# Kernel optimization log

Measured on AMD Instinct MI355X. Metric: run time of the kernel, lower is better.

Reference implementation:

```python
import jax, jax.numpy as jnp
import numpy as np

H = 2048      # hidden_size
DM = 4096     # intermediate_size
N = 16        # ssm state size
K = 4         # conv kernel
R = 128       # time_step_rank
B_SZ = 1
L = 1024


def setup_inputs() -> dict:
    key = jax.random.key(0)
    ks = jax.random.split(key, 10)
    s = 0.02
    hidden_states = jax.random.normal(ks[0], (B_SZ, L, H), dtype=jnp.float32)
    W_in = jax.random.normal(ks[1], (2 * DM, H), dtype=jnp.float32) * s
    conv_w = jax.random.normal(ks[2], (DM, 1, K), dtype=jnp.float32) * 0.3
    conv_b = jax.random.normal(ks[3], (DM,), dtype=jnp.float32) * 0.1
    W_x = jax.random.normal(ks[4], (R + 2 * N, DM), dtype=jnp.float32) * s
    W_dt = jax.random.normal(ks[5], (DM, R), dtype=jnp.float32) * s
    b_dt = jax.random.normal(ks[6], (DM,), dtype=jnp.float32) * 0.1
    # A_log init: log(arange(1..N)) broadcast over channels (per __init__)
    A_log = jnp.broadcast_to(jnp.log(jnp.arange(1, N + 1, dtype=jnp.float32))[None, :], (DM, N)).copy()
    D_param = jnp.ones((DM,), dtype=jnp.float32)
    W_out = jax.random.normal(ks[7], (H, DM), dtype=jnp.float32) * s
    return {"hidden_states": hidden_states, "W_in": W_in, "conv_w": conv_w,
            "conv_b": conv_b, "W_x": W_x, "W_dt": W_dt, "b_dt": b_dt,
            "A_log": A_log, "D_param": D_param, "W_out": W_out}


def reference(hidden_states, W_in, conv_w, conv_b, W_x, W_dt, b_dt, A_log, D_param, W_out):
    # in_proj then chunk into hidden / gate (torch chunks dim=1 after transpose)
    proj = hidden_states @ W_in.T                     # [B, L, 2D]
    h, gate = proj[..., :DM], proj[..., DM:]          # each [B, L, D]
    # depthwise causal conv1d, padding K-1 then truncate to L (left-pad == same)
    h_cl = jnp.transpose(h, (0, 2, 1))                # [B, D, L]
    hc = jax.lax.conv_general_dilated(
        h_cl, conv_w, window_strides=(1,), padding=[(K - 1, 0)],
        dimension_numbers=("NCH", "OIH", "NCH"), feature_group_count=DM)
    hc = jax.nn.silu(hc + conv_b[None, :, None])      # [B, D, L]
    hc_ld = jnp.transpose(hc, (0, 2, 1))              # [B, L, D]
    # x_proj -> dt, B, C
    ssm_p = hc_ld @ W_x.T                             # [B, L, R+2N]
    ts, Bm, Cm = ssm_p[..., :R], ssm_p[..., R:R + N], ssm_p[..., R + N:]
    dt = jax.nn.softplus(ts @ W_dt.T + b_dt)          # [B, L, D]
    A = -jnp.exp(A_log)                               # [D, N]
    dA = jnp.exp(dt[:, :, :, None] * A[None, None, :, :])            # [B, L, D, N]
    dBu = dt[:, :, :, None] * Bm[:, :, None, :] * hc_ld[:, :, :, None]  # [B, L, D, N]
    # selective scan over time: state = dA*state + dBu; y = <state, C>
    def step(state, inp):
        dA_t, dBu_t, C_t = inp                        # [B,D,N],[B,D,N],[B,N]
        state = dA_t * state + dBu_t
        y = jnp.einsum("bdn,bn->bd", state, C_t)
        return state, y
    init = jnp.zeros((hidden_states.shape[0], DM, N), dtype=hidden_states.dtype)
    _, ys = jax.lax.scan(step, init,
                         (jnp.swapaxes(dA, 0, 1), jnp.swapaxes(dBu, 0, 1), jnp.swapaxes(Cm, 0, 1)))
    y = jnp.transpose(ys, (1, 0, 2))                  # [B, L, D]
    y = y + hc_ld * D_param[None, None, :]            # skip via D
    y = y * jax.nn.silu(gate)                         # gating
    return y @ W_out.T                                # [B, L, H]
```

## Files before the change

### kernel.cpp

```cpp
#include <hip/hip_runtime.h>
#include <math.h>

#define AS1 __attribute__((address_space(1)))
#define AS3 __attribute__((address_space(3)))

typedef __attribute__((ext_vector_type(8))) short short8;
typedef __attribute__((ext_vector_type(4))) float f32x4;

#define WAITV(n) asm volatile("s_waitcnt vmcnt(" #n ")" ::: "memory")
#define BARRIER() asm volatile("s_barrier" ::: "memory")

static __device__ __forceinline__ unsigned short f2bf(float f) {
    unsigned u = __float_as_uint(f);
    unsigned r = (u + 0x7fffu + ((u >> 16) & 1u)) >> 16;
    return (unsigned short)r;
}

__global__ __launch_bounds__(256) void cvt_f32_bf16(const float* __restrict__ src,
                                                    unsigned short* __restrict__ dst,
                                                    int n4) {
    int i = blockIdx.x * 256 + threadIdx.x;
    int stride = gridDim.x * 256;
    for (; i < n4; i += stride) {
        float4 v = ((const float4*)src)[i];
        ushort4 o;
        o.x = f2bf(v.x); o.y = f2bf(v.y); o.z = f2bf(v.z); o.w = f2bf(v.w);
        ((ushort4*)dst)[i] = o;
    }
}

__global__ __launch_bounds__(256) void cvt_ts(const float* __restrict__ ssmp,
                                              unsigned short* __restrict__ ts) {
    int i = blockIdx.x * 256 + threadIdx.x;
    int t = i >> 5, c4 = (i & 31) * 4;
    float4 v = *(const float4*)&ssmp[t * 160 + c4];
    ushort4 o;
    o.x = f2bf(v.x); o.y = f2bf(v.y); o.z = f2bf(v.z); o.w = f2bf(v.w);
    *(ushort4*)&ts[t * 128 + c4] = o;
}

__global__ __launch_bounds__(256) void conv_silu(const float* __restrict__ h,
                                                 const float* __restrict__ cw,
                                                 const float* __restrict__ cb,
                                                 float* __restrict__ hc_f,
                                                 unsigned short* __restrict__ hc_bf) {
    int idx = blockIdx.x * 256 + threadIdx.x;
    int d = idx & 4095, t = idx >> 12;
    float acc = cb[d];
    float4 w = *(const float4*)&cw[d * 4];
    const float* wp = (const float*)&w;
#pragma unroll
    for (int k = 0; k < 4; ++k) {
        int tt = t + k - 3;
        if (tt >= 0) acc += h[tt * 4096 + d] * wp[k];
    }
    float s = acc / (1.f + __expf(-acc));
    hc_f[idx] = s;
    hc_bf[idx] = f2bf(s);
}

__global__ __launch_bounds__(256) void reduce4(const float* __restrict__ pA,
                                               const float* __restrict__ pB,
                                               float* __restrict__ out, int n4) {
    int i = blockIdx.x * 256 + threadIdx.x;
    int stride = gridDim.x * 256;
    const size_t MN4 = (size_t)1024 * 2048 / 4;
    for (; i < n4; i += stride) {
        float4 a = ((const float4*)pA)[i];
        float4 b = ((const float4*)pA)[i + MN4];
        float4 c = ((const float4*)pB)[i];
        float4 d = ((const float4*)pB)[i + MN4];
        float4 o;
        o.x = (a.x + b.x) + (c.x + d.x);
        o.y = (a.y + b.y) + (c.y + d.y);
        o.z = (a.z + b.z) + (c.z + d.z);
        o.w = (a.w + b.w) + (c.w + d.w);
        ((float4*)out)[i] = o;
    }
}

enum { P_SPLIT = 0, P_PART = 1 };

template <int EPI>
__global__ __launch_bounds__(512, 2)
void gemm8p(const short* __restrict__ A, const short* __restrict__ B,
            float* __restrict__ C0, float* __restrict__ C1,
            int N, int K, int kchunk) {
    __shared__ short lds[3 * 24576];

    const int tid = threadIdx.x;
    const int wv = tid >> 6, ln = tid & 63;
    const int lr = ln & 15, kg = ln >> 4;
    const int wm = wv >> 2, wn = wv & 3;

    const int nwg = gridDim.x;
    const int bid = blockIdx.x;
    const int swz = (bid & 7) * (nwg >> 3) + (bid >> 3);
    const int by = swz & 7, bx = swz >> 3;
    const int m0 = by * 128;
    const int n0 = bx * 256;
    const int kbeg = blockIdx.z * kchunk;
    const int NT = kchunk >> 6;

    f32x4 acc[4][4];
#pragma unroll
    for (int mi = 0; mi < 4; ++mi)
#pragma unroll
        for (int ni = 0; ni < 4; ++ni) acc[mi][ni] = (f32x4){0.f, 0.f, 0.f, 0.f};

    const short* Abase = A + (size_t)m0 * K + kbeg;
    const short* Bbase = B + (size_t)n0 * K + kbeg;

#define STAGE(kt, b)                                                          \
    {                                                                         \
        short* lbase = &lds[(b) * 24576];                                     \
        _Pragma("unroll")                                                     \
        for (int r = 0; r < 2; ++r) {                                         \
            int c = r * 512 + tid;                                            \
            int row = c >> 3, cb8 = (c & 7) << 4;                             \
            int scb = cb8 ^ ((row & 7) << 4);                                 \
            const short* src = Abase + (size_t)row * K + (kt) * 64 + (scb >> 1); \
            short* dst = lbase + (r * 512 + wv * 64) * 8;                     \
            __builtin_amdgcn_global_load_lds((const AS1 void*)src,            \
                                             (AS3 void*)dst, 16, 0, 0);       \
        }                                                                     \
        _Pragma("unroll")                                                     \
        for (int r = 0; r < 4; ++r) {                                         \
            int c = r * 512 + tid;                                            \
            int row = c >> 3, cb8 = (c & 7) << 4;                             \
            int scb = cb8 ^ ((row & 7) << 4);                                 \
            const short* src = Bbase + (size_t)row * K + (kt) * 64 + (scb >> 1); \
            short* dst = lbase + 8192 + (r * 512 + wv * 64) * 8;              \
            __builtin_amdgcn_global_load_lds((const AS1 void*)src,            \
                                             (AS3 void*)dst, 16, 0, 0);       \
        }                                                                     \
    }

    STAGE(0, 0);
    if (NT > 1) STAGE(1, 1);

    for (int kt = 0; kt < NT; ++kt) {
        const int b = kt % 3;
        if (kt + 2 < NT) STAGE(kt + 2, (kt + 2) % 3);
        int ahead = NT - 1 - kt;
        if (ahead > 2) ahead = 2;
        if (ahead == 2) { WAITV(12); } else if (ahead == 1) { WAITV(6); } else { WAITV(0); }
        BARRIER();
        {
            const short* la = &lds[b * 24576];
            const short* lb = la + 8192;
#pragma unroll
            for (int ks = 0; ks < 2; ++ks) {
                short8 av[4], bv[4];
#pragma unroll
                for (int mi = 0; mi < 4; ++mi) {
                    int row = wm * 64 + mi * 16 + lr;
                    int col = (ks * 32 + kg * 8) ^ ((row & 7) << 3);
                    av[mi] = *(const short8*)&la[row * 64 + col];
                }
#pragma unroll
                for (int ni = 0; ni < 4; ++ni) {
                    int row = wn * 64 + ni * 16 + lr;
                    int col = (ks * 32 + kg * 8) ^ ((row & 7) << 3);
                    bv[ni] = *(const short8*)&lb[row * 64 + col];
                }
                __builtin_amdgcn_s_setprio(1);
#pragma unroll
                for (int mi = 0; mi < 4; ++mi)
#pragma unroll
                    for (int ni = 0; ni < 4; ++ni)
                        acc[mi][ni] = __builtin_amdgcn_mfma_f32_16x16x32_bf16(
                            av[mi], bv[ni], acc[mi][ni], 0, 0, 0);
                __builtin_amdgcn_s_setprio(0);
            }
        }
        BARRIER();
    }
#undef STAGE

#pragma unroll
    for (int mi = 0; mi < 4; ++mi) {
        int crow0 = m0 + wm * 64 + mi * 16 + kg * 4;
#pragma unroll
        for (int ni = 0; ni < 4; ++ni) {
            int ccol = n0 + wn * 64 + ni * 16 + lr;
#pragma unroll
            for (int i = 0; i < 4; ++i) {
                float v = acc[mi][ni][i];
                size_t crow = (size_t)(crow0 + i);
                if constexpr (EPI == P_SPLIT) {
                    if (ccol < 4096) C0[crow * 4096 + ccol] = v;
                    else C1[crow * 4096 + (ccol - 4096)] = v;
                } else {
                    float* Cz = (blockIdx.z < 2 ? C0 : C1) +
                                (size_t)(blockIdx.z & 1) * 1024 * 2048;
                    Cz[crow * N + ccol] = v;
                }
            }
        }
    }
}

enum { EPI_PLAIN = 0, EPI_SPLIT = 1, EPI_ATOMIC = 2, EPI_SOFTPLUS = 3 };

template <int BM, int EPI>
__global__ __launch_bounds__(256)
void gemm_bt(const short* __restrict__ A, const short* __restrict__ B,
             float* __restrict__ C, float* __restrict__ C2,
             const float* __restrict__ bias,
             int M, int N, int K, int ldc, int kcLen) {
    __shared__ short A_lds[BM * 32];
    __shared__ short B_lds[128 * 32];
    const int tid = threadIdx.x;
    const int wv = tid >> 6, ln = tid & 63;
    const int lr = ln & 15, kg = ln >> 4;
    const int m0 = blockIdx.y * BM;
    const int n0 = blockIdx.x * 128;
    const int kbeg = blockIdx.z * kcLen;
    const int kend = kbeg + kcLen;
    const int wm = wv >> 1, wn = wv & 1;
    constexpr int MR = BM / 32;

    f32x4 acc[MR][4];
#pragma unroll
    for (int mi = 0; mi < MR; ++mi)
#pragma unroll
        for (int ni = 0; ni < 4; ++ni) acc[mi][ni] = (f32x4){0.f, 0.f, 0.f, 0.f};

    const int arow = tid >> 2;
    const int kq8 = (tid & 3) * 8;

    for (int k0 = kbeg; k0 < kend; k0 += 32) {
#pragma unroll
        for (int r = 0; r < BM / 64; ++r) {
            const short* srcA = A + (size_t)(m0 + r * 64 + arow) * K + (k0 + kq8);
            short* dstA = &A_lds[(r * 64 + wv * 16) * 32];
            __builtin_amdgcn_global_load_lds((const AS1 void*)srcA, (AS3 void*)dstA, 16, 0, 0);
        }
#pragma unroll
        for (int r = 0; r < 2; ++r) {
            int brow = n0 + r * 64 + arow;
            if (brow > N - 1) brow = N - 1;
            const short* srcB = B + (size_t)brow * K + (k0 + kq8);
            short* dstB = &B_lds[(r * 64 + wv * 16) * 32];
            __builtin_amdgcn_global_load_lds((const AS1 void*)srcB, (AS3 void*)dstB, 16, 0, 0);
        }
        __syncthreads();

        short8 av[MR], bv[4];
#pragma unroll
        for (int mi = 0; mi < MR; ++mi)
            av[mi] = *(const short8*)&A_lds[(wm * (BM / 2) + mi * 16 + lr) * 32 + kg * 8];
#pragma unroll
        for (int ni = 0; ni < 4; ++ni)
            bv[ni] = *(const short8*)&B_lds[(wn * 64 + ni * 16 + lr) * 32 + kg * 8];
#pragma unroll
        for (int mi = 0; mi < MR; ++mi)
#pragma unroll
            for (int ni = 0; ni < 4; ++ni)
                acc[mi][ni] = __builtin_amdgcn_mfma_f32_16x16x32_bf16(av[mi], bv[ni], acc[mi][ni], 0, 0, 0);
        __syncthreads();
    }

#pragma unroll
    for (int mi = 0; mi < MR; ++mi) {
        int crow0 = m0 + wm * (BM / 2) + mi * 16 + kg * 4;
#pragma unroll
        for (int ni = 0; ni < 4; ++ni) {
            int ccol = n0 + wn * 64 + ni * 16 + lr;
#pragma unroll
            for (int i = 0; i < 4; ++i) {
                float v = acc[mi][ni][i];
                size_t crow = (size_t)(crow0 + i);
                if constexpr (EPI == EPI_PLAIN) {
                    C[crow * ldc + ccol] = v;
                } else if constexpr (EPI == EPI_SPLIT) {
                    if (ccol < 4096) C[crow * 4096 + ccol] = v;
                    else C2[crow * 4096 + (ccol - 4096)] = v;
                } else if constexpr (EPI == EPI_ATOMIC) {
                    if (ccol < N) atomicAdd(&C[crow * ldc + ccol], v);
                } else {
                    float x = v + bias[ccol];
                    C[crow * ldc + ccol] = fmaxf(x, 0.f) + log1pf(__expf(-fabsf(x)));
                }
            }
        }
    }
}

#define CLEN 16
#define NCH 64

__global__ __launch_bounds__(256)
void scan_p1(const float* __restrict__ dt, const float* __restrict__ hc,
             const float* __restrict__ ssmp, const float* __restrict__ A_log,
             float* __restrict__ Sbuf, float* __restrict__ dtsum) {
    const int tid = threadIdx.x;
    const int c = blockIdx.x & (NCH - 1);
    const int db = blockIdx.x >> 6;
    const int d = db * 256 + tid;
    const int t0 = c * CLEN;

    float Ac[16];
#pragma unroll
    for (int i = 0; i < 4; ++i) {
        float4 v = *(const float4*)&A_log[d * 16 + i * 4];
        Ac[i*4+0] = -__expf(v.x); Ac[i*4+1] = -__expf(v.y);
        Ac[i*4+2] = -__expf(v.z); Ac[i*4+3] = -__expf(v.w);
    }

    __shared__ float sB[CLEN][16];
    sB[tid >> 4][tid & 15] = ssmp[(t0 + (tid >> 4)) * 160 + 128 + (tid & 15)];
    __syncthreads();

    float st[16];
#pragma unroll
    for (int n = 0; n < 16; ++n) st[n] = 0.f;
    float ds = 0.f;

    for (int tt = 0; tt < CLEN; ++tt) {
        float dtv = dt[(size_t)(t0 + tt) * 4096 + d];
        float hcv = hc[(size_t)(t0 + tt) * 4096 + d];
        float du = dtv * hcv;
        ds += dtv;
#pragma unroll
        for (int n = 0; n < 16; ++n) {
            float dA = __expf(dtv * Ac[n]);
            st[n] = fmaf(dA, st[n], du * sB[tt][n]);
        }
    }

    float* o = Sbuf + ((size_t)c * 4096 + d) * 16;
#pragma unroll
    for (int i = 0; i < 4; ++i)
        *(float4*)&o[i * 4] = make_float4(st[i*4], st[i*4+1], st[i*4+2], st[i*4+3]);
    dtsum[c * 4096 + d] = ds;
}

__global__ __launch_bounds__(256)
void scan_p2(const float* __restrict__ A_log, const float* __restrict__ dtsum,
             float* __restrict__ S) {
    const int idx = blockIdx.x * 256 + threadIdx.x;
    const int d = idx >> 4;
    const float Ac = -__expf(A_log[idx]);

    float sl[NCH], Pv[NCH];
#pragma unroll
    for (int c = 0; c < NCH; ++c) sl[c] = S[(size_t)c * 65536 + idx];
#pragma unroll
    for (int c = 0; c < NCH; ++c) Pv[c] = __expf(Ac * dtsum[c * 4096 + d]);

    float s = 0.f;
#pragma unroll
    for (int c = 0; c < NCH; ++c) {
        S[(size_t)c * 65536 + idx] = s;
        s = fmaf(Pv[c], s, sl[c]);
    }
}

__global__ __launch_bounds__(256)
void scan_p3(const float* __restrict__ dt, const float* __restrict__ hc,
             const float* __restrict__ ssmp, const float* __restrict__ A_log,
             const float* __restrict__ Dp, const float* __restrict__ gate,
             const float* __restrict__ Sinit, unsigned short* __restrict__ y_bf) {
    const int tid = threadIdx.x;
    const int c = blockIdx.x & (NCH - 1);
    const int db = blockIdx.x >> 6;
    const int d = db * 256 + tid;
    const int t0 = c * CLEN;

    float Ac[16];
#pragma unroll
    for (int i = 0; i < 4; ++i) {
        float4 v = *(const float4*)&A_log[d * 16 + i * 4];
        Ac[i*4+0] = -__expf(v.x); Ac[i*4+1] = -__expf(v.y);
        Ac[i*4+2] = -__expf(v.z); Ac[i*4+3] = -__expf(v.w);
    }
    const float Dcoef = Dp[d];

    __shared__ float sB[CLEN][16], sC[CLEN][16];
    {
        int tt = tid >> 4, nn = tid & 15;
        sB[tt][nn] = ssmp[(t0 + tt) * 160 + 128 + nn];
        sC[tt][nn] = ssmp[(t0 + tt) * 160 + 144 + nn];
    }
    __syncthreads();

    float st[16];
    {
        const float* si = Sinit + ((size_t)c * 4096 + d) * 16;
#pragma unroll
        for (int i = 0; i < 4; ++i) {
            float4 v = *(const float4*)&si[i * 4];
            st[i*4] = v.x; st[i*4+1] = v.y; st[i*4+2] = v.z; st[i*4+3] = v.w;
        }
    }

    for (int tt = 0; tt < CLEN; ++tt) {
        size_t g = (size_t)(t0 + tt) * 4096 + d;
        float dtv = dt[g];
        float hcv = hc[g];
        float du = dtv * hcv;
        float p[16];
#pragma unroll
        for (int n = 0; n < 16; ++n) {
            float dA = __expf(dtv * Ac[n]);
            st[n] = fmaf(dA, st[n], du * sB[tt][n]);
            p[n] = st[n] * sC[tt][n];
        }
#pragma unroll
        for (int n = 0; n < 8; ++n) p[n] += p[n + 8];
#pragma unroll
        for (int n = 0; n < 4; ++n) p[n] += p[n + 4];
        p[0] += p[2]; p[1] += p[3];
        float csum = p[0] + p[1];
        float gv = gate[g];
        float yv = (csum + hcv * Dcoef) * (gv / (1.f + __expf(-gv)));
        y_bf[g] = f2bf(yv);
    }
}

extern "C" void kernel_launch(void* const* d_in, const int* in_sizes, int n_in,
                              void* d_out, int out_size, void* d_ws, size_t ws_size,
                              hipStream_t stream) {
    (void)in_sizes; (void)n_in; (void)out_size; (void)ws_size;
    const float* hidden = (const float*)d_in[0];
    const float* W_in   = (const float*)d_in[1];
    const float* conv_w = (const float*)d_in[2];
    const float* conv_b = (const float*)d_in[3];
    const float* W_x    = (const float*)d_in[4];
    const float* W_dt   = (const float*)d_in[5];
    const float* b_dt   = (const float*)d_in[6];
    const float* A_log  = (const float*)d_in[7];
    const float* D_p    = (const float*)d_in[8];
    const float* W_out  = (const float*)d_in[9];
    float* out = (float*)d_out;

    char* w = (char*)d_ws;
    unsigned short* hid_bf = (unsigned short*)w;  w += (size_t)1024 * 2048 * 2;
    unsigned short* Wbig   = (unsigned short*)w;  w += (size_t)8192 * 2048 * 2;
    float* h_buf           = (float*)w;           w += (size_t)1024 * 4096 * 4;
    float* gate            = (float*)w;           w += (size_t)1024 * 4096 * 4;
    float* hc_f            = (float*)w;           w += (size_t)1024 * 4096 * 4;
    unsigned short* hc_bf  = (unsigned short*)w;  w += (size_t)1024 * 4096 * 2;
    float* ssmp            = (float*)w;           w += (size_t)1024 * 160 * 4;
    unsigned short* ts_bf  = (unsigned short*)w;  w += (size_t)1024 * 128 * 2;
    unsigned short* Wx_bf  = (unsigned short*)w;  w += (size_t)160 * 4096 * 2;
    unsigned short* Wdt_bf = (unsigned short*)w;  w += (size_t)4096 * 128 * 2;
    unsigned short* y_bf   = (unsigned short*)w;  w += (size_t)1024 * 4096 * 2;
    float* Sbuf            = (float*)w;           w += (size_t)NCH * 4096 * 16 * 4;
    float* dtsum           = (float*)w;           w += (size_t)NCH * 4096 * 4;

    hipMemsetAsync(ssmp, 0, (size_t)1024 * 160 * 4, stream);

    cvt_f32_bf16<<<2048, 256, 0, stream>>>(hidden, hid_bf, 1024 * 2048 / 4);
    cvt_f32_bf16<<<4096, 256, 0, stream>>>(W_in, Wbig, 8192 * 2048 / 4);
    cvt_f32_bf16<<<640, 256, 0, stream>>>(W_x, Wx_bf, 160 * 4096 / 4);
    cvt_f32_bf16<<<512, 256, 0, stream>>>(W_dt, Wdt_bf, 4096 * 128 / 4);

    gemm8p<P_SPLIT><<<dim3(256, 1, 1), 512, 0, stream>>>(
        (const short*)hid_bf, (const short*)Wbig, h_buf, gate, 8192, 2048, 2048);

    conv_silu<<<16384, 256, 0, stream>>>(h_buf, conv_w, conv_b, hc_f, hc_bf);

    cvt_f32_bf16<<<2048, 256, 0, stream>>>(W_out, Wbig, 2048 * 4096 / 4);

    gemm_bt<128, EPI_ATOMIC><<<dim3(2, 8, 16), 256, 0, stream>>>(
        (const short*)hc_bf, (const short*)Wx_bf, ssmp, nullptr, nullptr,
        1024, 160, 4096, 160, 256);

    cvt_ts<<<128, 256, 0, stream>>>(ssmp, ts_bf);

    gemm_bt<128, EPI_SOFTPLUS><<<dim3(32, 8, 1), 256, 0, stream>>>(
        (const short*)ts_bf, (const short*)Wdt_bf, h_buf, nullptr, b_dt,
        1024, 4096, 128, 4096, 128);

    scan_p1<<<NCH * 16, 256, 0, stream>>>(h_buf, hc_f, ssmp, A_log, Sbuf, dtsum);
    scan_p2<<<256, 256, 0, stream>>>(A_log, dtsum, Sbuf);
    scan_p3<<<NCH * 16, 256, 0, stream>>>(h_buf, hc_f, ssmp, A_log, D_p, gate, Sbuf, y_bf);

    gemm8p<P_PART><<<dim3(64, 1, 4), 512, 0, stream>>>(
        (const short*)y_bf, (const short*)Wbig, Sbuf, hc_f, 2048, 4096, 1024);
    reduce4<<<2048, 256, 0, stream>>>(Sbuf, hc_f, out, 1024 * 2048 / 4);
}
```

Measured before the change: 220.4 us.

## Store intermediates in bf16, fuse gate SiLU into GEMM, interleave GEMM prefetch

```diff
diff --git a/kernel.cpp b/kernel.cpp
--- a/kernel.cpp
+++ b/kernel.cpp
@@ -8,12 +8,17 @@
 typedef __attribute__((ext_vector_type(4))) float f32x4;
 
 #define WAITV(n) asm volatile("s_waitcnt vmcnt(" #n ")" ::: "memory")
+#define LGKM0()  asm volatile("s_waitcnt lgkmcnt(0)" ::: "memory")
 #define BARRIER() asm volatile("s_barrier" ::: "memory")
+#define SCHEDB() __builtin_amdgcn_sched_barrier(0)
 
 static __device__ __forceinline__ unsigned short f2bf(float f) {
     unsigned u = __float_as_uint(f);
     unsigned r = (u + 0x7fffu + ((u >> 16) & 1u)) >> 16;
     return (unsigned short)r;
+}
+static __device__ __forceinline__ float bf2f(unsigned short u) {
+    return __uint_as_float(((unsigned)u) << 16);
 }
 
 __global__ __launch_bounds__(256) void cvt_f32_bf16(const float* __restrict__ src,
@@ -42,7 +47,6 @@
 __global__ __launch_bounds__(256) void conv_silu(const float* __restrict__ h,
                                                  const float* __restrict__ cw,
                                                  const float* __restrict__ cb,
-                                                 float* __restrict__ hc_f,
                                                  unsigned short* __restrict__ hc_bf) {
     int idx = blockIdx.x * 256 + threadIdx.x;
     int d = idx & 4095, t = idx >> 12;
@@ -55,7 +59,6 @@
         if (tt >= 0) acc += h[tt * 4096 + d] * wp[k];
     }
     float s = acc / (1.f + __expf(-acc));
-    hc_f[idx] = s;
     hc_bf[idx] = f2bf(s);
 }
 
@@ -79,12 +82,12 @@
     }
 }
 
-enum { P_SPLIT = 0, P_PART = 1 };
+enum { P_GATE = 0, P_PART = 1 };
 
 template <int EPI>
 __global__ __launch_bounds__(512, 2)
 void gemm8p(const short* __restrict__ A, const short* __restrict__ B,
-            float* __restrict__ C0, float* __restrict__ C1,
+            void* __restrict__ C0v, void* __restrict__ C1v,
             int N, int K, int kchunk) {
     __shared__ short lds[3 * 24576];
 
@@ -111,7 +114,7 @@
     const short* Abase = A + (size_t)m0 * K + kbeg;
     const short* Bbase = B + (size_t)n0 * K + kbeg;
 
-#define STAGE(kt, b)                                                          \
+#define STAGE_A(kt, b)                                                        \
     {                                                                         \
         short* lbase = &lds[(b) * 24576];                                     \
         _Pragma("unroll")                                                     \
@@ -124,8 +127,12 @@
             __builtin_amdgcn_global_load_lds((const AS1 void*)src,            \
                                              (AS3 void*)dst, 16, 0, 0);       \
         }                                                                     \
+    }
+#define STAGE_B(kt, b, r0)                                                    \
+    {                                                                         \
+        short* lbase = &lds[(b) * 24576];                                     \
         _Pragma("unroll")                                                     \
-        for (int r = 0; r < 4; ++r) {                                         \
+        for (int r = (r0); r < (r0) + 2; ++r) {                               \
             int c = r * 512 + tid;                                            \
             int row = c >> 3, cb8 = (c & 7) << 4;                             \
             int scb = cb8 ^ ((row & 7) << 4);                                 \
@@ -135,48 +142,67 @@
                                              (AS3 void*)dst, 16, 0, 0);       \
         }                                                                     \
     }
-
-    STAGE(0, 0);
-    if (NT > 1) STAGE(1, 1);
+#define RD_A(dst, mi, ks)                                                     \
+    { int row = wm * 64 + (mi) * 16 + lr;                                     \
+      int col = ((ks) * 32 + kg * 8) ^ ((row & 7) << 3);                      \
+      dst = *(const short8*)&la[row * 64 + col]; }
+#define RD_B(dst, ni, ks)                                                     \
+    { int row = wn * 64 + (ni) * 16 + lr;                                     \
+      int col = ((ks) * 32 + kg * 8) ^ ((row & 7) << 3);                      \
+      dst = *(const short8*)&lb[row * 64 + col]; }
+#define MFMA4(mi, a)                                                          \
+    acc[mi][0] = __builtin_amdgcn_mfma_f32_16x16x32_bf16(a, vb0, acc[mi][0], 0, 0, 0); \
+    acc[mi][1] = __builtin_amdgcn_mfma_f32_16x16x32_bf16(a, vb1, acc[mi][1], 0, 0, 0); \
+    acc[mi][2] = __builtin_amdgcn_mfma_f32_16x16x32_bf16(a, vb2, acc[mi][2], 0, 0, 0); \
+    acc[mi][3] = __builtin_amdgcn_mfma_f32_16x16x32_bf16(a, vb3, acc[mi][3], 0, 0, 0);
+
+    STAGE_A(0, 0); STAGE_B(0, 0, 0); STAGE_B(0, 0, 2);
+    if (NT > 1) { STAGE_A(1, 1); STAGE_B(1, 1, 0); STAGE_B(1, 1, 2); }
 
     for (int kt = 0; kt < NT; ++kt) {
         const int b = kt % 3;
-        if (kt + 2 < NT) STAGE(kt + 2, (kt + 2) % 3);
-        int ahead = NT - 1 - kt;
-        if (ahead > 2) ahead = 2;
-        if (ahead == 2) { WAITV(12); } else if (ahead == 1) { WAITV(6); } else { WAITV(0); }
+        const int bnx = (kt + 2) % 3;
+        const bool pf = (kt + 2 < NT);
+        if (kt + 1 < NT) { WAITV(6); } else { WAITV(0); }
         BARRIER();
-        {
-            const short* la = &lds[b * 24576];
-            const short* lb = la + 8192;
-#pragma unroll
-            for (int ks = 0; ks < 2; ++ks) {
-                short8 av[4], bv[4];
-#pragma unroll
-                for (int mi = 0; mi < 4; ++mi) {
-                    int row = wm * 64 + mi * 16 + lr;
-                    int col = (ks * 32 + kg * 8) ^ ((row & 7) << 3);
-                    av[mi] = *(const short8*)&la[row * 64 + col];
-                }
-#pragma unroll
-                for (int ni = 0; ni < 4; ++ni) {
-                    int row = wn * 64 + ni * 16 + lr;
-                    int col = (ks * 32 + kg * 8) ^ ((row & 7) << 3);
-                    bv[ni] = *(const short8*)&lb[row * 64 + col];
-                }
-                __builtin_amdgcn_s_setprio(1);
-#pragma unroll
-                for (int mi = 0; mi < 4; ++mi)
-#pragma unroll
-                    for (int ni = 0; ni < 4; ++ni)
-                        acc[mi][ni] = __builtin_amdgcn_mfma_f32_16x16x32_bf16(
-                            av[mi], bv[ni], acc[mi][ni], 0, 0, 0);
-                __builtin_amdgcn_s_setprio(0);
-            }
-        }
+        const short* la = &lds[b * 24576];
+        const short* lb = la + 8192;
+        short8 vb0, vb1, vb2, vb3, va0, va1;
+        RD_B(vb0, 0, 0); RD_B(vb1, 1, 0); RD_B(vb2, 2, 0); RD_B(vb3, 3, 0);
+        RD_A(va0, 0, 0); RD_A(va1, 1, 0);
+        if (pf) STAGE_A(kt + 2, bnx);
+        LGKM0(); SCHEDB();
+        __builtin_amdgcn_s_setprio(1);
+        MFMA4(0, va0); MFMA4(1, va1);
+        __builtin_amdgcn_s_setprio(0); SCHEDB();
         BARRIER();
-    }
-#undef STAGE
+        RD_A(va0, 2, 0); RD_A(va1, 3, 0);
+        if (pf) STAGE_B(kt + 2, bnx, 0);
+        LGKM0(); SCHEDB();
+        __builtin_amdgcn_s_setprio(1);
+        MFMA4(2, va0); MFMA4(3, va1);
+        __builtin_amdgcn_s_setprio(0); SCHEDB();
+        BARRIER();
+        RD_B(vb0, 0, 1); RD_B(vb1, 1, 1); RD_B(vb2, 2, 1); RD_B(vb3, 3, 1);
+        RD_A(va0, 0, 1); RD_A(va1, 1, 1);
+        if (pf) STAGE_B(kt + 2, bnx, 2);
+        LGKM0(); SCHEDB();
+        __builtin_amdgcn_s_setprio(1);
+        MFMA4(0, va0); MFMA4(1, va1);
+        __builtin_amdgcn_s_setprio(0); SCHEDB();
+        BARRIER();
+        RD_A(va0, 2, 1); RD_A(va1, 3, 1);
+        LGKM0(); SCHEDB();
+        __builtin_amdgcn_s_setprio(1);
+        MFMA4(2, va0); MFMA4(3, va1);
+        __builtin_amdgcn_s_setprio(0); SCHEDB();
+        BARRIER();
+    }
+#undef STAGE_A
+#undef STAGE_B
+#undef RD_A
+#undef RD_B
+#undef MFMA4
 
 #pragma unroll
     for (int mi = 0; mi < 4; ++mi) {
@@ -188,13 +214,16 @@
             for (int i = 0; i < 4; ++i) {
                 float v = acc[mi][ni][i];
                 size_t crow = (size_t)(crow0 + i);
-                if constexpr (EPI == P_SPLIT) {
-                    if (ccol < 4096) C0[crow * 4096 + ccol] = v;
-                    else C1[crow * 4096 + (ccol - 4096)] = v;
+                if constexpr (EPI == P_GATE) {
+                    if (ccol < 4096) ((float*)C0v)[crow * 4096 + ccol] = v;
+                    else {
+                        float s = v / (1.f + __expf(-v));
+                        ((unsigned short*)C1v)[crow * 4096 + (ccol - 4096)] = f2bf(s);
+                    }
                 } else {
-                    float* Cz = (blockIdx.z < 2 ? C0 : C1) +
-                                (size_t)(blockIdx.z & 1) * 1024 * 2048;
-                    Cz[crow * N + ccol] = v;
+                    float* P = (float*)(blockIdx.z < 2 ? C0v : C1v) +
+                               (size_t)(blockIdx.z & 1) * 1024 * 2048;
+                    P[crow * N + ccol] = v;
                 }
             }
         }
@@ -281,7 +310,8 @@
                     if (ccol < N) atomicAdd(&C[crow * ldc + ccol], v);
                 } else {
                     float x = v + bias[ccol];
-                    C[crow * ldc + ccol] = fmaxf(x, 0.f) + log1pf(__expf(-fabsf(x)));
+                    float sp = fmaxf(x, 0.f) + log1pf(__expf(-fabsf(x)));
+                    ((unsigned short*)C)[crow * ldc + ccol] = f2bf(sp);
                 }
             }
         }
@@ -292,7 +322,7 @@
 #define NCH 64
 
 __global__ __launch_bounds__(256)
-void scan_p1(const float* __restrict__ dt, const float* __restrict__ hc,
+void scan_p1(const unsigned short* __restrict__ dt, const unsigned short* __restrict__ hc,
              const float* __restrict__ ssmp, const float* __restrict__ A_log,
              float* __restrict__ Sbuf, float* __restrict__ dtsum) {
     const int tid = threadIdx.x;
@@ -319,8 +349,9 @@
     float ds = 0.f;
 
     for (int tt = 0; tt < CLEN; ++tt) {
-        float dtv = dt[(size_t)(t0 + tt) * 4096 + d];
-        float hcv = hc[(size_t)(t0 + tt) * 4096 + d];
+        size_t g = (size_t)(t0 + tt) * 4096 + d;
+        float dtv = bf2f(dt[g]);
+        float hcv = bf2f(hc[g]);
         float du = dtv * hcv;
         ds += dtv;
 #pragma unroll
@@ -359,9 +390,9 @@
 }
 
 __global__ __launch_bounds__(256)
-void scan_p3(const float* __restrict__ dt, const float* __restrict__ hc,
+void scan_p3(const unsigned short* __restrict__ dt, const unsigned short* __restrict__ hc,
              const float* __restrict__ ssmp, const float* __restrict__ A_log,
-             const float* __restrict__ Dp, const float* __restrict__ gate,
+             const float* __restrict__ Dp, const unsigned short* __restrict__ gate,
              const float* __restrict__ Sinit, unsigned short* __restrict__ y_bf) {
     const int tid = threadIdx.x;
     const int c = blockIdx.x & (NCH - 1);
@@ -398,8 +429,8 @@
 
     for (int tt = 0; tt < CLEN; ++tt) {
         size_t g = (size_t)(t0 + tt) * 4096 + d;
-        float dtv = dt[g];
-        float hcv = hc[g];
+        float dtv = bf2f(dt[g]);
+        float hcv = bf2f(hc[g]);
         float du = dtv * hcv;
         float p[16];
 #pragma unroll
@@ -414,8 +445,8 @@
         for (int n = 0; n < 4; ++n) p[n] += p[n + 4];
         p[0] += p[2]; p[1] += p[3];
         float csum = p[0] + p[1];
-        float gv = gate[g];
-        float yv = (csum + hcv * Dcoef) * (gv / (1.f + __expf(-gv)));
+        float gv = bf2f(gate[g]);
+        float yv = (csum + hcv * Dcoef) * gv;
         y_bf[g] = f2bf(yv);
     }
 }
@@ -440,9 +471,9 @@
     unsigned short* hid_bf = (unsigned short*)w;  w += (size_t)1024 * 2048 * 2;
     unsigned short* Wbig   = (unsigned short*)w;  w += (size_t)8192 * 2048 * 2;
     float* h_buf           = (float*)w;           w += (size_t)1024 * 4096 * 4;
-    float* gate            = (float*)w;           w += (size_t)1024 * 4096 * 4;
-    float* hc_f            = (float*)w;           w += (size_t)1024 * 4096 * 4;
+    unsigned short* gate_bf= (unsigned short*)w;  w += (size_t)1024 * 4096 * 2;
     unsigned short* hc_bf  = (unsigned short*)w;  w += (size_t)1024 * 4096 * 2;
+    unsigned short* dt_bf  = (unsigned short*)w;  w += (size_t)1024 * 4096 * 2;
     float* ssmp            = (float*)w;           w += (size_t)1024 * 160 * 4;
     unsigned short* ts_bf  = (unsigned short*)w;  w += (size_t)1024 * 128 * 2;
     unsigned short* Wx_bf  = (unsigned short*)w;  w += (size_t)160 * 4096 * 2;
@@ -458,10 +489,10 @@
     cvt_f32_bf16<<<640, 256, 0, stream>>>(W_x, Wx_bf, 160 * 4096 / 4);
     cvt_f32_bf16<<<512, 256, 0, stream>>>(W_dt, Wdt_bf, 4096 * 128 / 4);
 
-    gemm8p<P_SPLIT><<<dim3(256, 1, 1), 512, 0, stream>>>(
-        (const short*)hid_bf, (const short*)Wbig, h_buf, gate, 8192, 2048, 2048);
-
-    conv_silu<<<16384, 256, 0, stream>>>(h_buf, conv_w, conv_b, hc_f, hc_bf);
+    gemm8p<P_GATE><<<dim3(256, 1, 1), 512, 0, stream>>>(
+        (const short*)hid_bf, (const short*)Wbig, h_buf, gate_bf, 8192, 2048, 2048);
+
+    conv_silu<<<16384, 256, 0, stream>>>(h_buf, conv_w, conv_b, hc_bf);
 
     cvt_f32_bf16<<<2048, 256, 0, stream>>>(W_out, Wbig, 2048 * 4096 / 4);
 
@@ -472,14 +503,14 @@
     cvt_ts<<<128, 256, 0, stream>>>(ssmp, ts_bf);
 
     gemm_bt<128, EPI_SOFTPLUS><<<dim3(32, 8, 1), 256, 0, stream>>>(
-        (const short*)ts_bf, (const short*)Wdt_bf, h_buf, nullptr, b_dt,
+        (const short*)ts_bf, (const short*)Wdt_bf, (float*)dt_bf, nullptr, b_dt,
         1024, 4096, 128, 4096, 128);
 
-    scan_p1<<<NCH * 16, 256, 0, stream>>>(h_buf, hc_f, ssmp, A_log, Sbuf, dtsum);
+    scan_p1<<<NCH * 16, 256, 0, stream>>>(dt_bf, hc_bf, ssmp, A_log, Sbuf, dtsum);
     scan_p2<<<256, 256, 0, stream>>>(A_log, dtsum, Sbuf);
-    scan_p3<<<NCH * 16, 256, 0, stream>>>(h_buf, hc_f, ssmp, A_log, D_p, gate, Sbuf, y_bf);
+    scan_p3<<<NCH * 16, 256, 0, stream>>>(dt_bf, hc_bf, ssmp, A_log, D_p, gate_bf, Sbuf, y_bf);
 
     gemm8p<P_PART><<<dim3(64, 1, 4), 512, 0, stream>>>(
-        (const short*)y_bf, (const short*)Wbig, Sbuf, hc_f, 2048, 4096, 1024);
-    reduce4<<<2048, 256, 0, stream>>>(Sbuf, hc_f, out, 1024 * 2048 / 4);
-}
+        (const short*)y_bf, (const short*)Wbig, Sbuf, h_buf, 2048, 4096, 1024);
+    reduce4<<<2048, 256, 0, stream>>>(Sbuf, h_buf, out, 1024 * 2048 / 4);
+}
```

After: 216.2 us. Within noise of the previous version (-1.9%).
